# Kernel optimization log

Hardware: AMD Instinct MI355X
Metric: run time of the kernel (lower is better)

The kernel has to match this reference:

```python
import jax, jax.numpy as jnp
import numpy as np

SHAPES = ((64, 64), (32, 32), (16, 16), (8, 8))
LEVEL_STARTS = np.concatenate([[0], np.cumsum([h * w for h, w in SHAPES])]).tolist()
N_LEVELS = 4; N_HEADS = 8; N_POINTS = 4; D_MODEL = 256; HEAD_DIM = 32; D_FFN = 1024; NUM_LAYERS = 2
LEN_IN = sum(h * w for h, w in SHAPES)
BATCH = 2


def setup_inputs():
    key = jax.random.key(0)
    ks = iter(jax.random.split(key, 40))
    r = lambda shape, s=1.0: jax.random.normal(next(ks), shape, dtype=jnp.float32) * s
    L = NUM_LAYERS
    return {
        "src": r((BATCH, LEN_IN, D_MODEL)),
        "pos": r((BATCH, LEN_IN, D_MODEL), 0.5),
        "valid_ratios": jnp.ones((BATCH, N_LEVELS, 2), jnp.float32),
        "Wv": r((L, D_MODEL, D_MODEL), 0.05), "bv": jnp.zeros((L, D_MODEL), jnp.float32),
        "Woff": r((L, D_MODEL, N_HEADS * N_LEVELS * N_POINTS * 2), 0.002),
        "boff": r((L, N_HEADS * N_LEVELS * N_POINTS * 2), 0.5),
        "Wa": r((L, D_MODEL, N_HEADS * N_LEVELS * N_POINTS), 0.05),
        "ba": jnp.zeros((L, N_HEADS * N_LEVELS * N_POINTS), jnp.float32),
        "Wo": r((L, D_MODEL, D_MODEL), 0.05), "bo": jnp.zeros((L, D_MODEL), jnp.float32),
        "g1": jnp.ones((L, D_MODEL), jnp.float32), "be1": jnp.zeros((L, D_MODEL), jnp.float32),
        "Wl1": r((L, D_MODEL, D_FFN), 0.05), "bl1": jnp.zeros((L, D_FFN), jnp.float32),
        "Wl2": r((L, D_FFN, D_MODEL), 0.05), "bl2": jnp.zeros((L, D_MODEL), jnp.float32),
        "g2": jnp.ones((L, D_MODEL), jnp.float32), "be2": jnp.zeros((L, D_MODEL), jnp.float32),
    }


def layer_norm(x, g, b, eps=1e-5):
    m = jnp.mean(x, -1, keepdims=True)
    v = jnp.mean(jnp.square(x - m), -1, keepdims=True)
    return (x - m) * jax.lax.rsqrt(v + eps) * g + b


def make_reference_points(valid_ratios):
    # DeformableTransformerEncoder.get_reference_points, vectorized per level
    refs = []
    for lvl, (H, W) in enumerate(SHAPES):
        gy, gx = jnp.meshgrid(jnp.arange(H, dtype=jnp.float32) + 0.5,
                              jnp.arange(W, dtype=jnp.float32) + 0.5, indexing="ij")
        ry = gy.reshape(-1)[None] / (valid_ratios[:, lvl, 1][:, None] * H)
        rx = gx.reshape(-1)[None] / (valid_ratios[:, lvl, 0][:, None] * W)
        refs.append(jnp.stack([rx, ry], -1))  # [N, H*W, 2]
    ref = jnp.concatenate(refs, 1)  # [N, Len, 2]
    return ref[:, :, None, :] * valid_ratios[:, None]  # [N, Len, n_levels, 2]


def ms_deform_attn(query, input_flatten, reference_points, Wv, bv, Woff, boff, Wa, ba, Wo, bo):
    N, Lq, _ = query.shape
    value = (input_flatten @ Wv + bv).reshape(N, -1, N_HEADS, HEAD_DIM)
    off = (query @ Woff + boff).reshape(N, Lq, N_HEADS, N_LEVELS, N_POINTS, 2)
    aw = (query @ Wa + ba).reshape(N, Lq, N_HEADS, N_LEVELS * N_POINTS)
    aw = jax.nn.softmax(aw, -1).reshape(N, Lq, N_HEADS, N_LEVELS, N_POINTS)
    # normalizer is (W, H) per level, as in MSDeformAttn
    normalizer = jnp.array([[w, h] for h, w in SHAPES], jnp.float32)
    loc = reference_points[:, :, None, :, None, :] + off / normalizer[None, None, None, :, None, :]
    acc = jnp.zeros((N, N_HEADS, Lq, HEAD_DIM), query.dtype)
    for lvl, (H, W) in enumerate(SHAPES):
        s = LEVEL_STARTS[lvl]
        val = value[:, s:s + H * W].transpose(0, 2, 1, 3)  # [N, heads, H*W, hd]
        # grid_sample bilinear, align_corners=False, zero padding
        x = loc[:, :, :, lvl, :, 0] * W - 0.5  # [N, Lq, heads, P]
        y = loc[:, :, :, lvl, :, 1] * H - 0.5
        x0 = jnp.floor(x); y0 = jnp.floor(y)
        wx1 = x - x0; wy1 = y - y0
        ix0 = x0.astype(jnp.int32); iy0 = y0.astype(jnp.int32)

        def corner(ix, iy, w):
            valid = (ix >= 0) & (ix < W) & (iy >= 0) & (iy < H)
            idx = jnp.clip(iy, 0, H - 1) * W + jnp.clip(ix, 0, W - 1)
            idx = idx.transpose(0, 2, 1, 3).reshape(N, N_HEADS, Lq * N_POINTS)
            g = jnp.take_along_axis(val, idx[..., None], axis=2).reshape(N, N_HEADS, Lq, N_POINTS, HEAD_DIM)
            w = jnp.where(valid, w, 0.0).transpose(0, 2, 1, 3)  # [N, heads, Lq, P]
            return g * w[..., None]

        sampled = (corner(ix0, iy0, (1 - wx1) * (1 - wy1))
                   + corner(ix0 + 1, iy0, wx1 * (1 - wy1))
                   + corner(ix0, iy0 + 1, (1 - wx1) * wy1)
                   + corner(ix0 + 1, iy0 + 1, wx1 * wy1))
        acc = acc + (sampled * aw[:, :, :, lvl].transpose(0, 2, 1, 3)[..., None]).sum(3)
    out = acc.transpose(0, 2, 1, 3).reshape(N, Lq, D_MODEL)
    return out @ Wo + bo


def reference(src, pos, valid_ratios, Wv, bv, Woff, boff, Wa, ba, Wo, bo,
              g1, be1, Wl1, bl1, Wl2, bl2, g2, be2):
    ref_pts = make_reference_points(valid_ratios)
    out = src
    for l in range(NUM_LAYERS):
        q = out + pos  # with_pos_embed
        attn = ms_deform_attn(q, out, ref_pts, Wv[l], bv[l], Woff[l], boff[l],
                              Wa[l], ba[l], Wo[l], bo[l])
        out = layer_norm(out + attn, g1[l], be1[l])
        ffn = jax.nn.relu(out @ Wl1[l] + bl1[l]) @ Wl2[l] + bl2[l]
        out = layer_norm(out + ffn, g2[l], be2[l])
    return out
```

## Files before the change

### kernel.cpp

```cpp
#include <hip/hip_runtime.h>
#include <math.h>

#define LEN   5440
#define NB    2
#define MROWS (NB * LEN)
#define DM    256
#define NH    8
#define HD    32
#define NLV   4
#define NPT   4
#define DFFN  1024

typedef __attribute__((ext_vector_type(8))) short bf16x8;
typedef __attribute__((ext_vector_type(4))) short bf16x4;
typedef __attribute__((ext_vector_type(4))) float f32x4;

__device__ __forceinline__ short f2bf(float f) {
    union { float f; unsigned u; } cv; cv.f = f;
    unsigned r = cv.u + 0x7fffu + ((cv.u >> 16) & 1u);
    return (short)(r >> 16);
}
__device__ __forceinline__ float bf2f(short s) {
    union { unsigned u; float f; } cv;
    cv.u = ((unsigned)(unsigned short)s) << 16;
    return cv.f;
}

__global__ __launch_bounds__(256) void transpose_convert_all(
    const float* __restrict__ Wv,  const float* __restrict__ Woff,
    const float* __restrict__ Wa,  const float* __restrict__ Wo,
    const float* __restrict__ Wl1, const float* __restrict__ Wl2,
    short* __restrict__ out)
{
    int bx = blockIdx.x;
    int l  = bx / 736;
    int t  = bx % 736;
    const float* src; int K, N; long doff;
    if      (t < 64)  { src = Wv;   K = 256;  N = 256;  doff = 0;      }
    else if (t < 128) { src = Woff; K = 256;  N = 256;  doff = 65536;  t -= 64;  }
    else if (t < 160) { src = Wa;   K = 256;  N = 128;  doff = 131072; t -= 128; }
    else if (t < 224) { src = Wo;   K = 256;  N = 256;  doff = 163840; t -= 160; }
    else if (t < 480) { src = Wl1;  K = 256;  N = 1024; doff = 229376; t -= 224; }
    else              { src = Wl2;  K = 1024; N = 256;  doff = 491520; t -= 480; }
    src += (long)l * K * N;
    short* dst = out + (long)l * 753664 + doff;

    const int ntx = N / 32;
    const int n0 = (t % ntx) * 32, k0 = (t / ntx) * 32;

    __shared__ short T[32][33];
    const int tid = threadIdx.x;
    {
        const int n = tid & 31, kq = tid >> 5;
        #pragma unroll
        for (int i = 0; i < 4; ++i) {
            int k = kq * 4 + i;
            T[n][k] = f2bf(src[(long)(k0 + k) * N + n0 + n]);
        }
    }
    __syncthreads();
    {
        const int k = tid & 31, nq = tid >> 5;
        #pragma unroll
        for (int i = 0; i < 4; ++i) {
            int n = nq * 4 + i;
            dst[(long)(n0 + n) * K + k0 + k] = T[n][k];
        }
    }
}

__global__ __launch_bounds__(256) void convert_src(
    const float4* __restrict__ s4, const float4* __restrict__ p4,
    bf16x4* __restrict__ curb, bf16x4* __restrict__ qb)
{
    const int i = blockIdx.x * 256 + threadIdx.x;
    float4 s = s4[i], p = p4[i];
    bf16x4 c, q;
    c[0] = f2bf(s.x); c[1] = f2bf(s.y); c[2] = f2bf(s.z); c[3] = f2bf(s.w);
    q[0] = f2bf(s.x + p.x); q[1] = f2bf(s.y + p.y);
    q[2] = f2bf(s.z + p.z); q[3] = f2bf(s.w + p.w);
    curb[i] = c; qb[i] = q;
}

template <int BN, int RELU, int OMODE>
__device__ __forceinline__ void gemm_core128(
    short* As, short* Bs,
    const short* __restrict__ A, const short* __restrict__ Wt,
    const float* __restrict__ bias, float* __restrict__ Cf,
    short* __restrict__ Cb,
    int ldc, int m0, int wrow0, int ccol0, int K)
{
    constexpr int NF = BN / 32;
    constexpr int NBJ = BN / 64;
    const int t    = threadIdx.x;
    const int wave = t >> 6, lane = t & 63;
    const int wm   = (wave & 1) * 64;
    const int wn   = (wave >> 1) * (BN / 2);
    const int lm   = lane & 15;
    const int chkg = lane >> 4;
    const int srow = t >> 2;
    const int sc   = t & 3;

    f32x4 acc[4][NF] = {};
    bf16x8 ar[2], br[NBJ];

    #pragma unroll
    for (int j = 0; j < 2; ++j)
        ar[j] = *(const bf16x8*)(A + (long)(m0 + srow + 64 * j) * K + sc * 8);
    #pragma unroll
    for (int j = 0; j < NBJ; ++j)
        br[j] = *(const bf16x8*)(Wt + (long)(wrow0 + srow + 64 * j) * K + sc * 8);

    for (int k0 = 0; k0 < K; k0 += 32) {
        __syncthreads();
        #pragma unroll
        for (int j = 0; j < 2; ++j)
            *(bf16x8*)(&As[(srow + 64 * j) * 40 + sc * 8]) = ar[j];
        #pragma unroll
        for (int j = 0; j < NBJ; ++j)
            *(bf16x8*)(&Bs[(srow + 64 * j) * 40 + sc * 8]) = br[j];
        __syncthreads();

        if (k0 + 32 < K) {
            #pragma unroll
            for (int j = 0; j < 2; ++j)
                ar[j] = *(const bf16x8*)(A + (long)(m0 + srow + 64 * j) * K + k0 + 32 + sc * 8);
            #pragma unroll
            for (int j = 0; j < NBJ; ++j)
                br[j] = *(const bf16x8*)(Wt + (long)(wrow0 + srow + 64 * j) * K + k0 + 32 + sc * 8);
        }

        bf16x8 af[4], bfv[NF];
        #pragma unroll
        for (int s = 0; s < 4; ++s)
            af[s] = *(const bf16x8*)(&As[(wm + s * 16 + lm) * 40 + chkg * 8]);
        #pragma unroll
        for (int u = 0; u < NF; ++u)
            bfv[u] = *(const bf16x8*)(&Bs[(wn + u * 16 + lm) * 40 + chkg * 8]);
        #pragma unroll
        for (int s = 0; s < 4; ++s)
            #pragma unroll
            for (int u = 0; u < NF; ++u)
                acc[s][u] = __builtin_amdgcn_mfma_f32_16x16x32_bf16(
                    af[s], bfv[u], acc[s][u], 0, 0, 0);
    }

    const int col = lane & 15;
    const int rq  = (lane >> 4) * 4;
    #pragma unroll
    for (int s = 0; s < 4; ++s) {
        #pragma unroll
        for (int u = 0; u < NF; ++u) {
            const int gn = ccol0 + wn + u * 16 + col;
            const float bb = bias[gn];
            #pragma unroll
            for (int r = 0; r < 4; ++r) {
                const int gm = m0 + wm + s * 16 + rq + r;
                float v = acc[s][u][r] + bb;
                if (RELU) v = fmaxf(v, 0.f);
                if (OMODE == 0) {
                    Cf[(long)gm * ldc + gn] = v;
                } else if (OMODE == 1) {
                    Cb[(long)gm * ldc + gn] = f2bf(v);
                } else {
                    const int n   = gm / LEN;
                    const int pix = gm - n * LEN;
                    const int h   = gn >> 5, d = gn & 31;
                    Cb[((long)(n * NH + h) * LEN + pix) * 32 + d] = f2bf(v);
                }
            }
        }
    }
}

template <int BN, int RELU, int OMODE>
__global__ __launch_bounds__(256) void gemm128(
    const short* __restrict__ A, const short* __restrict__ Wt,
    const float* __restrict__ bias, float* Cf, short* Cb, int ldc, int K)
{
    __shared__ __align__(16) short As[128 * 40];
    __shared__ __align__(16) short Bs[BN * 40];
    gemm_core128<BN, RELU, OMODE>(As, Bs, A, Wt, bias, Cf, Cb, ldc,
                                  blockIdx.y * 128, blockIdx.x * BN,
                                  blockIdx.x * BN, K);
}

__global__ __launch_bounds__(256) void gemm_qkv128(
    const short* __restrict__ curb, const short* __restrict__ qb,
    const short* __restrict__ Wt, const float* __restrict__ bv,
    const float* __restrict__ boff, const float* __restrict__ ba,
    short* __restrict__ Vb, float* __restrict__ OFF, float* __restrict__ AW)
{
    __shared__ __align__(16) short As[128 * 40];
    __shared__ __align__(16) short Bs[128 * 40];
    const int n0 = blockIdx.x * 128;
    if (n0 < 256) {
        gemm_core128<128, 0, 2>(As, Bs, curb, Wt, bv, (float*)nullptr, Vb,
                                256, blockIdx.y * 128, n0, n0, 256);
    } else if (n0 < 512) {
        gemm_core128<128, 0, 0>(As, Bs, qb, Wt, boff, OFF, (short*)nullptr,
                                256, blockIdx.y * 128, n0, n0 - 256, 256);
    } else {
        gemm_core128<128, 0, 0>(As, Bs, qb, Wt, ba, AW, (short*)nullptr,
                                128, blockIdx.y * 128, n0, n0 - 512, 256);
    }
}

template <int K>
__global__ __launch_bounds__(256) void gemm_ln(
    const short* __restrict__ A, const short* __restrict__ Wt,
    const float* __restrict__ bias, const float* __restrict__ resid,
    const float* __restrict__ g, const float* __restrict__ be,
    float* __restrict__ outf, short* __restrict__ outb,
    short* __restrict__ outq, const float* __restrict__ pos)
{
    __shared__ __align__(16) short As[64 * 72];
    __shared__ __align__(16) short Bs[256 * 72];
    __shared__ float red[4][64][2];

    const int t    = threadIdx.x;
    const int wave = t >> 6, lane = t & 63;
    const int wn   = wave * 64;
    const int lm   = lane & 15;
    const int chkg = lane >> 4;
    const int srow = t >> 2;
    const int sc   = t & 3;
    const int m0   = blockIdx.x * 64;

    f32x4 acc[4][4] = {};
    bf16x8 ar[2], br[8];

    #pragma unroll
    for (int c = 0; c < 2; ++c)
        ar[c] = *(const bf16x8*)(A + (long)(m0 + srow) * K + c * 32 + sc * 8);
    #pragma unroll
    for (int j = 0; j < 4; ++j)
        #pragma unroll
        for (int c = 0; c < 2; ++c)
            br[j * 2 + c] = *(const bf16x8*)(Wt + (long)(srow + 64 * j) * K + c * 32 + sc * 8);

    for (int k0 = 0; k0 < K; k0 += 64) {
        __syncthreads();
        #pragma unroll
        for (int c = 0; c < 2; ++c)
            *(bf16x8*)(&As[srow * 72 + c * 32 + sc * 8]) = ar[c];
        #pragma unroll
        for (int j = 0; j < 4; ++j)
            #pragma unroll
            for (int c = 0; c < 2; ++c)
                *(bf16x8*)(&Bs[(srow + 64 * j) * 72 + c * 32 + sc * 8]) = br[j * 2 + c];
        __syncthreads();

        if (k0 + 64 < K) {
            #pragma unroll
            for (int c = 0; c < 2; ++c)
                ar[c] = *(const bf16x8*)(A + (long)(m0 + srow) * K + k0 + 64 + c * 32 + sc * 8);
            #pragma unroll
            for (int j = 0; j < 4; ++j)
                #pragma unroll
                for (int c = 0; c < 2; ++c)
                    br[j * 2 + c] = *(const bf16x8*)(Wt + (long)(srow + 64 * j) * K + k0 + 64 + c * 32 + sc * 8);
        }

        #pragma unroll
        for (int kk = 0; kk < 2; ++kk) {
            bf16x8 af[4], bfv[4];
            #pragma unroll
            for (int s = 0; s < 4; ++s)
                af[s] = *(const bf16x8*)(&As[(s * 16 + lm) * 72 + kk * 32 + chkg * 8]);
            #pragma unroll
            for (int u = 0; u < 4; ++u)
                bfv[u] = *(const bf16x8*)(&Bs[(wn + u * 16 + lm) * 72 + kk * 32 + chkg * 8]);
            #pragma unroll
            for (int s = 0; s < 4; ++s)
                #pragma unroll
                for (int u = 0; u < 4; ++u)
                    acc[s][u] = __builtin_amdgcn_mfma_f32_16x16x32_bf16(
                        af[s], bfv[u], acc[s][u], 0, 0, 0);
        }
    }

    const int rq = (lane >> 4) * 4;
    #pragma unroll
    for (int u = 0; u < 4; ++u) {
        const int gn = wn + u * 16 + lm;
        const float bb = bias[gn];
        #pragma unroll
        for (int s = 0; s < 4; ++s)
            #pragma unroll
            for (int r = 0; r < 4; ++r)
                acc[s][u][r] += bb + resid[(long)(m0 + s * 16 + rq + r) * DM + gn];
    }

    float ps[4][4], p2[4][4];
    #pragma unroll
    for (int s = 0; s < 4; ++s)
        #pragma unroll
        for (int r = 0; r < 4; ++r) {
            float sm = 0.f, s2 = 0.f;
            #pragma unroll
            for (int u = 0; u < 4; ++u) {
                const float v = acc[s][u][r];
                sm += v; s2 += v * v;
            }
            ps[s][r] = sm; p2[s][r] = s2;
        }
    #pragma unroll
    for (int o = 1; o < 16; o <<= 1)
        #pragma unroll
        for (int s = 0; s < 4; ++s)
            #pragma unroll
            for (int r = 0; r < 4; ++r) {
                ps[s][r] += __shfl_xor(ps[s][r], o, 64);
                p2[s][r] += __shfl_xor(p2[s][r], o, 64);
            }
    if (lm == 0) {
        #pragma unroll
        for (int s = 0; s < 4; ++s)
            #pragma unroll
            for (int r = 0; r < 4; ++r) {
                red[wave][s * 16 + rq + r][0] = ps[s][r];
                red[wave][s * 16 + rq + r][1] = p2[s][r];
            }
    }
    __syncthreads();

    float mean[4][4], rstd[4][4];
    #pragma unroll
    for (int s = 0; s < 4; ++s)
        #pragma unroll
        for (int r = 0; r < 4; ++r) {
            const int row = s * 16 + rq + r;
            const float ts = red[0][row][0] + red[1][row][0] + red[2][row][0] + red[3][row][0];
            const float t2 = red[0][row][1] + red[1][row][1] + red[2][row][1] + red[3][row][1];
            const float m = ts * (1.f / DM);
            mean[s][r] = m;
            rstd[s][r] = rsqrtf(t2 * (1.f / DM) - m * m + 1e-5f);
        }

    #pragma unroll
    for (int u = 0; u < 4; ++u) {
        const int gn = wn + u * 16 + lm;
        const float gg = g[gn], bbe = be[gn];
        #pragma unroll
        for (int s = 0; s < 4; ++s)
            #pragma unroll
            for (int r = 0; r < 4; ++r) {
                const long gm = m0 + s * 16 + rq + r;
                const float o = (acc[s][u][r] - mean[s][r]) * rstd[s][r] * gg + bbe;
                outf[gm * DM + gn] = o;
                if (outb) outb[gm * DM + gn] = f2bf(o);
                if (outq) outq[gm * DM + gn] = f2bf(o + pos[gm * DM + gn]);
            }
    }
}

__global__ __launch_bounds__(256) void deform_attn_v3(
    const short* __restrict__ Vb,
    const float* __restrict__ OFF,
    const float* __restrict__ AW,
    const float* __restrict__ vr,
    bf16x4* __restrict__ ATTb)
{
    const int starts[5] = {0, 4096, 5120, 5376, 5440};
    const int dims[4]   = {64, 32, 16, 8};

    const int wave = threadIdx.x >> 6;
    const int lane = threadIdx.x & 63;
    const int h    = lane >> 3;
    const int d4   = lane & 7;

    const int gq = blockIdx.x * 4 + wave;
    const int n  = gq / LEN;
    const int q  = gq % LEN;

    int lq = 3;
    if (q < 4096) lq = 0; else if (q < 5120) lq = 1; else if (q < 5376) lq = 2;
    const int r  = q - starts[lq];
    const int Wq = dims[lq];
    const int gy = r / Wq, gx = r % Wq;
    const float vrxq = vr[(n * NLV + lq) * 2 + 0];
    const float vryq = vr[(n * NLV + lq) * 2 + 1];
    const float rx = (gx + 0.5f) / (vrxq * Wq);
    const float ry = (gy + 0.5f) / (vryq * Wq);

    const long row = (long)n * LEN + q;

    const float* awp = AW + row * 128 + h * 16;
    float a[16];
    float mx = -1e30f;
    #pragma unroll
    for (int i = 0; i < 16; ++i) { a[i] = awp[i]; mx = fmaxf(mx, a[i]); }
    float s = 0.f;
    #pragma unroll
    for (int i = 0; i < 16; ++i) { a[i] = __expf(a[i] - mx); s += a[i]; }
    const float inv = 1.f / s;

    const float* offp = OFF + row * 256 + h * 32;

    float4 acc = {0.f, 0.f, 0.f, 0.f};
    #pragma unroll
    for (int lvl = 0; lvl < NLV; ++lvl) {
        const int Hl = dims[lvl];
        const int Wl = Hl;
        const float fW = (float)Wl;
        const int sb = starts[lvl];
        const float lx = rx * vr[(n * NLV + lvl) * 2 + 0];
        const float ly = ry * vr[(n * NLV + lvl) * 2 + 1];
        const short* vb = Vb + ((long)(n * NH + h) * LEN + sb) * 32 + d4 * 4;
        #pragma unroll
        for (int p = 0; p < NPT; ++p) {
            const float ox = offp[lvl * 8 + p * 2 + 0];
            const float oy = offp[lvl * 8 + p * 2 + 1];
            const float x = fmaf(lx, fW, ox) - 0.5f;
            const float y = fmaf(ly, fW, oy) - 0.5f;
            const float x0f = floorf(x), y0f = floorf(y);
            const int ix0 = (int)x0f, iy0 = (int)y0f;
            const float wx1 = x - x0f, wy1 = y - y0f;
            const float wx0 = 1.f - wx1, wy0 = 1.f - wy1;

            const bool vx0 = (ix0 >= 0)     && (ix0 < Wl);
            const bool vx1 = (ix0 + 1 >= 0) && (ix0 + 1 < Wl);
            const bool vy0 = (iy0 >= 0)     && (iy0 < Hl);
            const bool vy1 = (iy0 + 1 >= 0) && (iy0 + 1 < Hl);
            const int cx0 = min(max(ix0, 0), Wl - 1);
            const int cx1 = min(max(ix0 + 1, 0), Wl - 1);
            const int cy0 = min(max(iy0, 0), Hl - 1);
            const int cy1 = min(max(iy0 + 1, 0), Hl - 1);

            const float w00 = (vx0 && vy0) ? wx0 * wy0 : 0.f;
            const float w10 = (vx1 && vy0) ? wx1 * wy0 : 0.f;
            const float w01 = (vx0 && vy1) ? wx0 * wy1 : 0.f;
            const float w11 = (vx1 && vy1) ? wx1 * wy1 : 0.f;

            const bf16x4 g00 = *(const bf16x4*)(vb + (long)(cy0 * Wl + cx0) * 32);
            const bf16x4 g10 = *(const bf16x4*)(vb + (long)(cy0 * Wl + cx1) * 32);
            const bf16x4 g01 = *(const bf16x4*)(vb + (long)(cy1 * Wl + cx0) * 32);
            const bf16x4 g11 = *(const bf16x4*)(vb + (long)(cy1 * Wl + cx1) * 32);

            const float awv = a[lvl * 4 + p] * inv;
            #pragma unroll
            for (int e = 0; e < 4; ++e) {
                float sv = w00 * bf2f(g00[e]) + w10 * bf2f(g10[e])
                         + w01 * bf2f(g01[e]) + w11 * bf2f(g11[e]);
                (&acc.x)[e] += awv * sv;
            }
        }
    }
    bf16x4 ob;
    ob[0] = f2bf(acc.x); ob[1] = f2bf(acc.y);
    ob[2] = f2bf(acc.z); ob[3] = f2bf(acc.w);
    ATTb[row * 64 + h * 8 + d4] = ob;
}

extern "C" void kernel_launch(void* const* d_in, const int* in_sizes, int n_in,
                              void* d_out, int out_size, void* d_ws, size_t ws_size,
                              hipStream_t stream)
{
    const float* src = (const float*)d_in[0];
    const float* pos = (const float*)d_in[1];
    const float* vr  = (const float*)d_in[2];
    const float* Wv_   = (const float*)d_in[3];
    const float* bv_   = (const float*)d_in[4];
    const float* Woff_ = (const float*)d_in[5];
    const float* boff_ = (const float*)d_in[6];
    const float* Wa_   = (const float*)d_in[7];
    const float* ba_   = (const float*)d_in[8];
    const float* Wo_   = (const float*)d_in[9];
    const float* bo_   = (const float*)d_in[10];
    const float* g1_   = (const float*)d_in[11];
    const float* be1_  = (const float*)d_in[12];
    const float* Wl1_  = (const float*)d_in[13];
    const float* bl1_  = (const float*)d_in[14];
    const float* Wl2_  = (const float*)d_in[15];
    const float* bl2_  = (const float*)d_in[16];
    const float* g2_   = (const float*)d_in[17];
    const float* be2_  = (const float*)d_in[18];

    const long SZ = (long)MROWS * DM;
    float* ws = (float*)d_ws;
    float* OFF  = ws;
    float* AW   = OFF + SZ;
    float* XA   = AW  + (long)MROWS * 128;
    float* XB   = XA  + SZ;
    short* Vb   = (short*)(XB + SZ);
    short* curb = Vb   + SZ;
    short* qb   = curb + SZ;
    short* ATTb = qb   + SZ;
    short* XAb  = ATTb + SZ;
    short* FFNb = XAb  + SZ;
    short* Wt   = FFNb + (long)MROWS * DFFN;

    const dim3 blk(256);
    const int GYM = MROWS / 128;
    const int GLN = MROWS / 64;

    hipLaunchKernelGGL(transpose_convert_all, dim3(1472), blk, 0, stream,
                       Wv_, Woff_, Wa_, Wo_, Wl1_, Wl2_, Wt);
    hipLaunchKernelGGL(convert_src, dim3(SZ / 4 / 256), blk, 0, stream,
                       (const float4*)src, (const float4*)pos,
                       (bf16x4*)curb, (bf16x4*)qb);

    const float* cur = src;
    for (int l = 0; l < 2; ++l) {
        const short* Wbase = Wt + (long)l * 753664;
        const float* bv   = bv_   + (long)l * DM;
        const float* boff = boff_ + (long)l * 256;
        const float* ba   = ba_   + (long)l * 128;
        const float* bo   = bo_   + (long)l * DM;
        const float* g1   = g1_   + (long)l * DM;
        const float* be1  = be1_  + (long)l * DM;
        const float* bl1  = bl1_  + (long)l * DFFN;
        const float* bl2  = bl2_  + (long)l * DM;
        const float* g2   = g2_   + (long)l * DM;
        const float* be2  = be2_  + (long)l * DM;

        hipLaunchKernelGGL(gemm_qkv128, dim3(5, GYM), blk, 0, stream,
                           curb, qb, Wbase, bv, boff, ba, Vb, OFF, AW);
        hipLaunchKernelGGL(deform_attn_v3, dim3(MROWS / 4), blk, 0, stream,
                           Vb, OFF, AW, vr, (bf16x4*)ATTb);
        hipLaunchKernelGGL((gemm_ln<256>), dim3(GLN), blk, 0, stream,
                           ATTb, Wbase + 163840, bo, cur, g1, be1,
                           XA, XAb, (short*)nullptr, (const float*)nullptr);
        hipLaunchKernelGGL((gemm128<128, 1, 1>), dim3(8, GYM), blk, 0, stream,
                           XAb, Wbase + 229376, bl1, (float*)nullptr, FFNb, 1024, 256);
        if (l == 0) {
            hipLaunchKernelGGL((gemm_ln<1024>), dim3(GLN), blk, 0, stream,
                               FFNb, Wbase + 491520, bl2, XA, g2, be2,
                               XB, curb, qb, pos);
            cur = XB;
        } else {
            hipLaunchKernelGGL((gemm_ln<1024>), dim3(GLN), blk, 0, stream,
                               FFNb, Wbase + 491520, bl2, XA, g2, be2,
                               (float*)d_out, (short*)nullptr, (short*)nullptr,
                               (const float*)nullptr);
        }
    }
}
```

Measured before the change: 319.9 us.

## Fuse FFN up-projection, ReLU, down-projection and LayerNorm into one kernel

Replaces the separate FFN1 GEMM (writing a bf16 hidden buffer to global memory) and the FFN2+LayerNorm kernel with a single kernel. Each 32-row block computes the 1024-wide hidden activation in two 512-column halves kept in shared memory and accumulates the down-projection directly. The intent is to remove the global round trip of the MROWS x 1024 intermediate and one launch per layer. In exchange, weights are read straight from global memory without LDS tiling, and each block is small (32 rows) with large shared memory use, which may limit occupancy and weight reuse.

New measurement: 360.2 us. +12.6%, slower.

```diff
diff --git a/kernel.cpp b/kernel.cpp
--- a/kernel.cpp
+++ b/kernel.cpp
@@ -14,6 +14,8 @@
 typedef __attribute__((ext_vector_type(8))) short bf16x8;
 typedef __attribute__((ext_vector_type(4))) short bf16x4;
 typedef __attribute__((ext_vector_type(4))) float f32x4;
+
+#define MFMA16 __builtin_amdgcn_mfma_f32_16x16x32_bf16
 
 __device__ __forceinline__ short f2bf(float f) {
     union { float f; unsigned u; } cv; cv.f = f;
@@ -141,8 +143,7 @@
         for (int s = 0; s < 4; ++s)
             #pragma unroll
             for (int u = 0; u < NF; ++u)
-                acc[s][u] = __builtin_amdgcn_mfma_f32_16x16x32_bf16(
-                    af[s], bfv[u], acc[s][u], 0, 0, 0);
+                acc[s][u] = MFMA16(af[s], bfv[u], acc[s][u], 0, 0, 0);
     }
 
     const int col = lane & 15;
@@ -173,18 +174,6 @@
     }
 }
 
-template <int BN, int RELU, int OMODE>
-__global__ __launch_bounds__(256) void gemm128(
-    const short* __restrict__ A, const short* __restrict__ Wt,
-    const float* __restrict__ bias, float* Cf, short* Cb, int ldc, int K)
-{
-    __shared__ __align__(16) short As[128 * 40];
-    __shared__ __align__(16) short Bs[BN * 40];
-    gemm_core128<BN, RELU, OMODE>(As, Bs, A, Wt, bias, Cf, Cb, ldc,
-                                  blockIdx.y * 128, blockIdx.x * BN,
-                                  blockIdx.x * BN, K);
-}
-
 __global__ __launch_bounds__(256) void gemm_qkv128(
     const short* __restrict__ curb, const short* __restrict__ qb,
     const short* __restrict__ Wt, const float* __restrict__ bv,
@@ -275,8 +264,7 @@
             for (int s = 0; s < 4; ++s)
                 #pragma unroll
                 for (int u = 0; u < 4; ++u)
-                    acc[s][u] = __builtin_amdgcn_mfma_f32_16x16x32_bf16(
-                        af[s], bfv[u], acc[s][u], 0, 0, 0);
+                    acc[s][u] = MFMA16(af[s], bfv[u], acc[s][u], 0, 0, 0);
         }
     }
 
@@ -344,6 +332,161 @@
         const float gg = g[gn], bbe = be[gn];
         #pragma unroll
         for (int s = 0; s < 4; ++s)
+            #pragma unroll
+            for (int r = 0; r < 4; ++r) {
+                const long gm = m0 + s * 16 + rq + r;
+                const float o = (acc[s][u][r] - mean[s][r]) * rstd[s][r] * gg + bbe;
+                outf[gm * DM + gn] = o;
+                if (outb) outb[gm * DM + gn] = f2bf(o);
+                if (outq) outq[gm * DM + gn] = f2bf(o + pos[gm * DM + gn]);
+            }
+    }
+}
+
+__global__ __launch_bounds__(256) void ffn_fused(
+    const short* __restrict__ XAb,
+    const short* __restrict__ Wl1t,
+    const short* __restrict__ Wl2t,
+    const float* __restrict__ bl1, const float* __restrict__ bl2,
+    const float* __restrict__ resid,
+    const float* __restrict__ g, const float* __restrict__ be,
+    float* __restrict__ outf, short* __restrict__ outb,
+    short* __restrict__ outq, const float* __restrict__ pos)
+{
+    __shared__ __align__(16) short Xs[32 * 264];
+    __shared__ __align__(16) short Hs[32 * 520];
+    __shared__ float red[4][32][2];
+
+    const int t    = threadIdx.x;
+    const int wave = t >> 6, lane = t & 63;
+    const int lm   = lane & 15;
+    const int chkg = lane >> 4;
+    const int m0   = blockIdx.x * 32;
+
+    {
+        const bf16x8* src = (const bf16x8*)(XAb + (long)m0 * 256);
+        #pragma unroll
+        for (int j = 0; j < 4; ++j) {
+            const int linear = t + 256 * j;
+            const int m = linear >> 5, kv = (linear & 31) * 8;
+            *(bf16x8*)(&Xs[m * 264 + kv]) = src[linear];
+        }
+    }
+
+    f32x4 acc[2][4] = {};
+
+    for (int hh = 0; hh < 2; ++hh) {
+        __syncthreads();
+
+        bf16x8 af1[2][8];
+        #pragma unroll
+        for (int s = 0; s < 2; ++s)
+            #pragma unroll
+            for (int k0 = 0; k0 < 8; ++k0)
+                af1[s][k0] = *(const bf16x8*)(&Xs[(s * 16 + lm) * 264 + k0 * 32 + chkg * 8]);
+
+        const int hwb = hh * 512 + wave * 128;
+        #pragma unroll
+        for (int nc = 0; nc < 8; ++nc) {
+            f32x4 a1[2] = {};
+            const short* wrow = Wl1t + (long)(hwb + nc * 16 + lm) * 256 + chkg * 8;
+            #pragma unroll
+            for (int k0 = 0; k0 < 8; ++k0) {
+                const bf16x8 bf = *(const bf16x8*)(wrow + k0 * 32);
+                a1[0] = MFMA16(af1[0][k0], bf, a1[0], 0, 0, 0);
+                a1[1] = MFMA16(af1[1][k0], bf, a1[1], 0, 0, 0);
+            }
+            const int hcol_l = wave * 128 + nc * 16 + lm;
+            const float bb = bl1[hwb + nc * 16 + lm];
+            #pragma unroll
+            for (int s = 0; s < 2; ++s)
+                #pragma unroll
+                for (int r = 0; r < 4; ++r) {
+                    const float v = fmaxf(a1[s][r] + bb, 0.f);
+                    Hs[(s * 16 + chkg * 4 + r) * 520 + hcol_l] = f2bf(v);
+                }
+        }
+        __syncthreads();
+
+        const short* w2base = Wl2t + (long)(wave * 64 + lm) * 1024 + hh * 512 + chkg * 8;
+        #pragma unroll 4
+        for (int k0 = 0; k0 < 16; ++k0) {
+            bf16x8 af[2];
+            af[0] = *(const bf16x8*)(&Hs[lm * 520        + k0 * 32 + chkg * 8]);
+            af[1] = *(const bf16x8*)(&Hs[(16 + lm) * 520 + k0 * 32 + chkg * 8]);
+            #pragma unroll
+            for (int u = 0; u < 4; ++u) {
+                const bf16x8 bf = *(const bf16x8*)(w2base + (long)u * 16 * 1024 + k0 * 32);
+                acc[0][u] = MFMA16(af[0], bf, acc[0][u], 0, 0, 0);
+                acc[1][u] = MFMA16(af[1], bf, acc[1][u], 0, 0, 0);
+            }
+        }
+    }
+
+    const int rq = chkg * 4;
+    #pragma unroll
+    for (int u = 0; u < 4; ++u) {
+        const int gn = wave * 64 + u * 16 + lm;
+        const float bb = bl2[gn];
+        #pragma unroll
+        for (int s = 0; s < 2; ++s)
+            #pragma unroll
+            for (int r = 0; r < 4; ++r)
+                acc[s][u][r] += bb + resid[(long)(m0 + s * 16 + rq + r) * DM + gn];
+    }
+
+    float ps[2][4], p2[2][4];
+    #pragma unroll
+    for (int s = 0; s < 2; ++s)
+        #pragma unroll
+        for (int r = 0; r < 4; ++r) {
+            float sm = 0.f, s2 = 0.f;
+            #pragma unroll
+            for (int u = 0; u < 4; ++u) {
+                const float v = acc[s][u][r];
+                sm += v; s2 += v * v;
+            }
+            ps[s][r] = sm; p2[s][r] = s2;
+        }
+    #pragma unroll
+    for (int o = 1; o < 16; o <<= 1)
+        #pragma unroll
+        for (int s = 0; s < 2; ++s)
+            #pragma unroll
+            for (int r = 0; r < 4; ++r) {
+                ps[s][r] += __shfl_xor(ps[s][r], o, 64);
+                p2[s][r] += __shfl_xor(p2[s][r], o, 64);
+            }
+    if (lm == 0) {
+        #pragma unroll
+        for (int s = 0; s < 2; ++s)
+            #pragma unroll
+            for (int r = 0; r < 4; ++r) {
+                red[wave][s * 16 + rq + r][0] = ps[s][r];
+                red[wave][s * 16 + rq + r][1] = p2[s][r];
+            }
+    }
+    __syncthreads();
+
+    float mean[2][4], rstd[2][4];
+    #pragma unroll
+    for (int s = 0; s < 2; ++s)
+        #pragma unroll
+        for (int r = 0; r < 4; ++r) {
+            const int row = s * 16 + rq + r;
+            const float ts = red[0][row][0] + red[1][row][0] + red[2][row][0] + red[3][row][0];
+            const float t2 = red[0][row][1] + red[1][row][1] + red[2][row][1] + red[3][row][1];
+            const float m = ts * (1.f / DM);
+            mean[s][r] = m;
+            rstd[s][r] = rsqrtf(t2 * (1.f / DM) - m * m + 1e-5f);
+        }
+
+    #pragma unroll
+    for (int u = 0; u < 4; ++u) {
+        const int gn = wave * 64 + u * 16 + lm;
+        const float gg = g[gn], bbe = be[gn];
+        #pragma unroll
+        for (int s = 0; s < 2; ++s)
             #pragma unroll
             for (int r = 0; r < 4; ++r) {
                 const long gm = m0 + s * 16 + rq + r;
@@ -488,12 +631,12 @@
     short* qb   = curb + SZ;
     short* ATTb = qb   + SZ;
     short* XAb  = ATTb + SZ;
-    short* FFNb = XAb  + SZ;
-    short* Wt   = FFNb + (long)MROWS * DFFN;
+    short* Wt   = XAb  + SZ;
 
     const dim3 blk(256);
     const int GYM = MROWS / 128;
     const int GLN = MROWS / 64;
+    const int GFF = MROWS / 32;
 
     hipLaunchKernelGGL(transpose_convert_all, dim3(1472), blk, 0, stream,
                        Wv_, Woff_, Wa_, Wo_, Wl1_, Wl2_, Wt);
@@ -522,18 +665,16 @@
         hipLaunchKernelGGL((gemm_ln<256>), dim3(GLN), blk, 0, stream,
                            ATTb, Wbase + 163840, bo, cur, g1, be1,
                            XA, XAb, (short*)nullptr, (const float*)nullptr);
-        hipLaunchKernelGGL((gemm128<128, 1, 1>), dim3(8, GYM), blk, 0, stream,
-                           XAb, Wbase + 229376, bl1, (float*)nullptr, FFNb, 1024, 256);
         if (l == 0) {
-            hipLaunchKernelGGL((gemm_ln<1024>), dim3(GLN), blk, 0, stream,
-                               FFNb, Wbase + 491520, bl2, XA, g2, be2,
-                               XB, curb, qb, pos);
+            hipLaunchKernelGGL(ffn_fused, dim3(GFF), blk, 0, stream,
+                               XAb, Wbase + 229376, Wbase + 491520, bl1, bl2,
+                               XA, g2, be2, XB, curb, qb, pos);
             cur = XB;
         } else {
-            hipLaunchKernelGGL((gemm_ln<1024>), dim3(GLN), blk, 0, stream,
-                               FFNb, Wbase + 491520, bl2, XA, g2, be2,
-                               (float*)d_out, (short*)nullptr, (short*)nullptr,
-                               (const float*)nullptr);
-        }
-    }
-}
+            hipLaunchKernelGGL(ffn_fused, dim3(GFF), blk, 0, stream,
+                               XAb, Wbase + 229376, Wbase + 491520, bl1, bl2,
+                               XA, g2, be2, (float*)d_out, (short*)nullptr,
+                               (short*)nullptr, (const float*)nullptr);
+        }
+    }
+}
```
